# Performance work log

Measured on AMD Instinct MI355X. Metric: run time of the kernel, lower is better.

Reference implementation:

```python
import jax, jax.numpy as jnp
import numpy as np

# model constants (ModelArgs defaults, 7B config)
H, D, BS = 32, 128, 8          # heads, head_dim, sparse_block_size
DIM = H * D                     # 4096
SINK_TOK, WIN_TOK, HEAVY = 60, 60, 1160
MB = HEAVY // BS                # 145 top blocks
T_CTX = 16384                   # prefilled context length


def apply_rope(x, freqs):
    # x: [B,S,H,D], freqs: [S, D//2, 2] -> rotate pairs as in apply_rotary_emb
    B, S, Hh, Dd = x.shape
    xs = x.reshape(B, S, Hh, Dd // 2, 2)
    fc = freqs.reshape(1, S, 1, Dd // 2, 2)
    xr, xi = xs[..., 0], xs[..., 1]
    fr, fi = fc[..., 0], fc[..., 1]
    out = jnp.stack([xr * fr - xi * fi, xi * fr + xr * fi], axis=-1)
    return out.reshape(B, S, Hh, Dd)


def setup_inputs() -> dict:
    key = jax.random.key(0)
    ks = jax.random.split(key, 6)
    B = 1
    return {
        'x': jax.random.normal(ks[0], (B, 1, DIM), jnp.float32),
        'freqs_cis': jax.random.normal(ks[1], (1, D // 2, 2), jnp.float32),
        'wqkv': jax.random.normal(ks[2], (3 * DIM, DIM), jnp.float32) * 0.02,
        'wo': jax.random.normal(ks[3], (DIM, DIM), jnp.float32) * 0.02,
        'k_cache': jax.random.normal(ks[4], (B, H, T_CTX, D), jnp.float32),
        'v_cache': jax.random.normal(ks[5], (B, H, T_CTX, D), jnp.float32),
        'input_pos': T_CTX - 1,
    }


def reference(x, freqs_cis, wqkv, wo, k_cache, v_cache, input_pos):
    B, S, _ = x.shape  # decode step, S == 1
    qkv = x @ wqkv.T                                   # [B,S,3*DIM]
    q, k, v = jnp.split(qkv, [DIM, 2 * DIM], axis=-1)
    q = q.reshape(B, S, H, D)
    k = k.reshape(B, S, H, D)
    v = v.reshape(B, S, H, D)
    q = apply_rope(q, freqs_cis)
    k = apply_rope(k, freqs_cis)

    # KV cache update at input_pos (token layout [B,H,T,D])
    k_bhsd = k.transpose(0, 2, 1, 3)
    v_bhsd = v.transpose(0, 2, 1, 3)
    kc = jax.lax.dynamic_update_slice(k_cache, k_bhsd, (0, 0, input_pos, 0))
    vc = jax.lax.dynamic_update_slice(v_cache, v_bhsd, (0, 0, input_pos, 0))

    T = input_pos + 1            # python int -> static
    Tb = T // BS                 # full blocks (T divisible by BS here)
    scale = 1.0 / np.sqrt(D).astype(np.float32)

    # block representative keys (k_sum_blk / k_cnt_blk mean) and routing scores
    k_mean = kc[:, :, :T].reshape(B, H, Tb, BS, D).mean(axis=3)   # [B,H,Tb,D]
    q1 = q[:, -1]                                                 # [B,H,D]
    scores = jnp.einsum('bhd,bhtd->bht', q1, k_mean) * scale      # [B,H,Tb]

    # build_block_index: sink + window + topk-Mb (static sizes)
    sink_b = min(-(-min(SINK_TOK, T) // BS), Tb)
    window_b = min(-(-min(WIN_TOK, T) // BS), Tb)
    cur_block = (T - 1) // BS
    win_start = max(0, cur_block - window_b + 1)
    win_end = cur_block + 1
    NEG = jnp.float32(-1e30)
    tb = jnp.arange(Tb)
    excl = (tb < sink_b) | ((tb >= win_start) & (tb < win_end))
    _, top_ids = jax.lax.top_k(jnp.where(excl, NEG, scores), MB)  # [B,H,MB]
    sink_ids = jnp.broadcast_to(jnp.arange(sink_b, dtype=jnp.int32), (B, H, sink_b))
    win_ids = jnp.broadcast_to(jnp.arange(win_start, win_end, dtype=jnp.int32), (B, H, win_end - win_start))
    block_index = jnp.concatenate([sink_ids, win_ids, top_ids.astype(jnp.int32)], axis=-1)  # [B,H,KLIST]

    # gather selected blocks' tokens and run restricted attention
    tok = (block_index[..., None] * BS + jnp.arange(BS, dtype=jnp.int32)).reshape(B, H, -1)  # [B,H,N]
    N = tok.shape[-1]
    valid = tok <= input_pos
    tok_c = jnp.clip(tok, 0, T - 1).astype(jnp.int32)
    idx = jnp.broadcast_to(tok_c[..., None], (B, H, N, D))
    k_sel = jnp.take_along_axis(kc, idx, axis=2)                  # [B,H,N,D]
    v_sel = jnp.take_along_axis(vc, idx, axis=2)
    att = jnp.einsum('bhd,bhnd->bhn', q1, k_sel) * scale
    p = jax.nn.softmax(jnp.where(valid, att, NEG), axis=-1)
    out = jnp.einsum('bhn,bhnd->bhd', p, v_sel)                   # [B,H,D]
    y = out.reshape(B, 1, DIM) @ wo.T                             # [B,1,DIM]
    return y
```

## Files before the change

### kernel.cpp

```cpp
#include <hip/hip_runtime.h>
#include <hip/hip_bf16.h>

#define NH 32
#define DH 128
#define DIMM 4096
#define TCTX 16384
#define BSZ 8
#define NBLK_TOT (TCTX / BSZ)
#define MB_SEL 145
#define SINK_TOK 60
#define WIN_TOK 60
#define BLK_CAP 192
#define NSPLIT 27
#define CHUNK 6
#define PSTRIDE (DH + 2)
#define KV_WGS 1024
#define SC_WG_PER_H 128
#define SC_WGS (NH * SC_WG_PER_H)

typedef __attribute__((ext_vector_type(4))) float f4v;

__device__ __forceinline__ float4 ntload4(const float* p) {
    f4v v = __builtin_nontemporal_load((const f4v*)p);
    return make_float4(v.x, v.y, v.z, v.w);
}

__device__ __forceinline__ void gemv_row2(const float* __restrict__ wr0,
                                          const float* __restrict__ wr1,
                                          const float* __restrict__ x, int lane,
                                          float& o0, float& o1) {
    float a0 = 0.f, a1 = 0.f;
    #pragma unroll
    for (int it = 0; it < 16; ++it) {
        int j = lane * 4 + it * 256;
        float4 xv = *(const float4*)(x + j);
        float4 w0 = ntload4(wr0 + j);
        float4 w1 = ntload4(wr1 + j);
        a0 += w0.x * xv.x + w0.y * xv.y + w0.z * xv.z + w0.w * xv.w;
        a1 += w1.x * xv.x + w1.y * xv.y + w1.z * xv.z + w1.w * xv.w;
    }
    #pragma unroll
    for (int m = 1; m < 64; m <<= 1) {
        a0 += __shfl_xor(a0, m, 64);
        a1 += __shfl_xor(a1, m, 64);
    }
    o0 = a0; o1 = a1;
}

__global__ __launch_bounds__(256) void k_q(const float* __restrict__ x,
                                           const float* __restrict__ w,
                                           const float* __restrict__ freqs,
                                           float* __restrict__ q1) {
    int t = threadIdx.x;
    int wave = t >> 6, lane = t & 63;
    int r0 = blockIdx.x * 8 + wave * 2;
    float a0, a1;
    gemv_row2(w + (size_t)r0 * DIMM, w + (size_t)(r0 + 1) * DIMM, x, lane, a0, a1);
    if (lane == 0) {
        int m = (r0 >> 1) & 63;
        float fr = freqs[2 * m], fi = freqs[2 * m + 1];
        float2 o; o.x = a0 * fr - a1 * fi; o.y = a1 * fr + a0 * fi;
        *(float2*)(q1 + r0) = o;
    }
}

__global__ __launch_bounds__(256) void k_mid(const float* __restrict__ x,
                                             const float* __restrict__ w,
                                             const float* __restrict__ freqs,
                                             const float* __restrict__ q1,
                                             const float* __restrict__ kc,
                                             const int* __restrict__ ip_p,
                                             float* __restrict__ kn,
                                             float* __restrict__ vn,
                                             float* __restrict__ scores) {
    int t = threadIdx.x, wave = t >> 6, lane = t & 63;

    if (blockIdx.x < KV_WGS) {
        int r0 = DIMM + blockIdx.x * 8 + wave * 2;
        float a0, a1;
        gemv_row2(w + (size_t)r0 * DIMM, w + (size_t)(r0 + 1) * DIMM, x, lane, a0, a1);
        if (lane == 0) {
            if (r0 < 2 * DIMM) {
                int m = (r0 >> 1) & 63;
                float fr = freqs[2 * m], fi = freqs[2 * m + 1];
                float2 o; o.x = a0 * fr - a1 * fi; o.y = a1 * fr + a0 * fi;
                *(float2*)(kn + (r0 - DIMM)) = o;
            } else {
                float2 o; o.x = a0; o.y = a1;
                *(float2*)(vn + (r0 - 2 * DIMM)) = o;
            }
        }
        return;
    }

    int ip = *ip_p;
    int T = ip + 1;
    int Tb = T / BSZ;
    int sidx = blockIdx.x - KV_WGS;
    int h = sidx >> 7;
    int wg = sidx & 127;
    int b0 = wg * 16 + wave * 4;
    int d0 = (lane * 4) & 127;
    float4 q4 = *(const float4*)(q1 + h * DH + d0);
    const float* kb = kc + ((size_t)h * TCTX + (size_t)b0 * BSZ) * DH;
    float acc[4] = {0.f, 0.f, 0.f, 0.f};
    #pragma unroll
    for (int i = 0; i < 16; ++i) {
        float4 k4 = *(const float4*)(kb + lane * 4 + i * 256);
        acc[i >> 2] += q4.x * k4.x + q4.y * k4.y + q4.z * k4.z + q4.w * k4.w;
    }
    #pragma unroll
    for (int m = 1; m < 64; m <<= 1) {
        acc[0] += __shfl_xor(acc[0], m, 64);
        acc[1] += __shfl_xor(acc[1], m, 64);
        acc[2] += __shfl_xor(acc[2], m, 64);
        acc[3] += __shfl_xor(acc[3], m, 64);
    }
    if (lane == 0) {
        float4 out;
        out.x = (b0 + 0 < Tb) ? acc[0] * 0.011048543456039805f : -1e30f;
        out.y = (b0 + 1 < Tb) ? acc[1] * 0.011048543456039805f : -1e30f;
        out.z = (b0 + 2 < Tb) ? acc[2] * 0.011048543456039805f : -1e30f;
        out.w = (b0 + 3 < Tb) ? acc[3] * 0.011048543456039805f : -1e30f;
        *(float4*)(scores + h * NBLK_TOT + b0) = out;
    }
}

__global__ __launch_bounds__(64) void k_topk(const float* __restrict__ scores,
                                             const int* __restrict__ ip_p,
                                             int* __restrict__ blklist) {
    int h = blockIdx.x;
    int lane = threadIdx.x & 63;
    int ip = *ip_p;
    int T = ip + 1;
    int Tb = T / BSZ;
    int sink_b = min((min(SINK_TOK, T) + BSZ - 1) / BSZ, Tb);
    int window_b = min((min(WIN_TOK, T) + BSZ - 1) / BSZ, Tb);
    int cur = (T - 1) / BSZ;
    int win_start = max(0, cur - window_b + 1);
    int win_end = cur + 1;

    unsigned int u[32];
    const float* sh = scores + h * NBLK_TOT;
    #pragma unroll
    for (int i = 0; i < 32; i += 4) {
        float4 sv = *(const float4*)(sh + lane * 32 + i);
        float fv[4] = {sv.x, sv.y, sv.z, sv.w};
        #pragma unroll
        for (int q = 0; q < 4; ++q) {
            int j = lane * 32 + i + q;
            unsigned int b = __float_as_uint(fv[q]);
            unsigned int m = (b & 0x80000000u) ? ~b : (b | 0x80000000u);
            bool ok = (j < Tb) && (j >= sink_b) && !(j >= win_start && j < win_end);
            u[i + q] = ok ? m : 0u;
        }
    }

    unsigned int lo = 0u, hi = 0xFFFFFFFFu;
    while (lo < hi) {
        unsigned int mid =
            (unsigned int)(((unsigned long long)lo + (unsigned long long)hi + 1ull) >> 1);
        int c = 0;
        #pragma unroll
        for (int i = 0; i < 32; ++i) c += (u[i] >= mid);
        #pragma unroll
        for (int m = 1; m < 64; m <<= 1) c += __shfl_xor(c, m, 64);
        if (c >= MB_SEL) lo = mid; else hi = mid - 1;
    }

    int gt = 0, eq = 0;
    #pragma unroll
    for (int i = 0; i < 32; ++i) { gt += (u[i] > lo); eq += (u[i] == lo); }
    unsigned int packed = ((unsigned int)gt << 16) | (unsigned int)eq;
    unsigned int sc = packed;
    #pragma unroll
    for (int off = 1; off < 64; off <<= 1) {
        unsigned int v = __shfl_up(sc, off, 64);
        if (lane >= off) sc += v;
    }
    unsigned int tot = __shfl(sc, 63, 64);
    unsigned int totg = tot >> 16;
    unsigned int excl = sc - packed;
    int gi = (int)(excl >> 16);
    int ei = (int)(excl & 0xFFFFu);
    int need_eq = MB_SEL - (int)totg;

    int base = sink_b + (win_end - win_start);
    int* bl = blklist + h * BLK_CAP;
    for (int i = lane; i < base; i += 64)
        bl[i] = (i < sink_b) ? i : (win_start + (i - sink_b));

    #pragma unroll
    for (int i = 0; i < 32; ++i) {
        int j = lane * 32 + i;
        if (u[i] > lo) {
            bl[base + gi] = j; ++gi;
        } else if (u[i] == lo) {
            if (ei < need_eq) bl[base + (int)totg + ei] = j;
            ++ei;
        }
    }
}

__global__ __launch_bounds__(256) void k_attn_part(const float* __restrict__ q1,
                                                   const float* __restrict__ kc,
                                                   const float* __restrict__ vc,
                                                   const float* __restrict__ kn,
                                                   const float* __restrict__ vn,
                                                   const int* __restrict__ blklist,
                                                   const int* __restrict__ ip_p,
                                                   float* __restrict__ part) {
    __shared__ float oacc[4][DH];
    __shared__ float2 ml_s[4];
    int h = blockIdx.x / NSPLIT;
    int sp = blockIdx.x % NSPLIT;
    int t = threadIdx.x, wave = t >> 6, lane = t & 63;
    int g = lane >> 4, sub = lane & 15;
    int ip = *ip_p;
    int T = ip + 1;
    int Tb = T / BSZ;
    int sink_b = min((min(SINK_TOK, T) + BSZ - 1) / BSZ, Tb);
    int window_b = min((min(WIN_TOK, T) + BSZ - 1) / BSZ, Tb);
    int cur = (T - 1) / BSZ;
    int win_start = max(0, cur - window_b + 1);
    int nwin = cur + 1 - win_start;
    int nblk = sink_b + nwin + MB_SEL;
    int b0 = sp * CHUNK;
    int nb = min(nblk - b0, CHUNK);
    float* pp = part + ((size_t)h * NSPLIT + sp) * PSTRIDE;
    if (nb <= 0) {
        if (t < DH) pp[t] = 0.f;
        if (t == DH) pp[DH] = -1e30f;
        if (t == DH + 1) pp[DH + 1] = 0.f;
        return;
    }

    float4 qa = *(const float4*)(q1 + h * DH + sub * 8);
    float4 qb = *(const float4*)(q1 + h * DH + sub * 8 + 4);
    const float* kh = kc + (size_t)h * TCTX * DH;
    const float* vh = vc + (size_t)h * TCTX * DH;
    const int* bl = blklist + h * BLK_CAP + b0;

    float m = -1e30f, l = 0.f;
    float4 aa = make_float4(0, 0, 0, 0), ab = make_float4(0, 0, 0, 0);

    for (int c = wave; c < nb * 2; c += 4) {
        int blk = bl[c >> 1];
        int tok = blk * BSZ + (c & 1) * 4 + g;
        const float* kr = (tok == ip) ? (kn + h * DH) : (kh + (size_t)tok * DH);
        const float* vr = (tok == ip) ? (vn + h * DH) : (vh + (size_t)tok * DH);
        float4 ka  = *(const float4*)(kr + sub * 8);
        float4 kb2 = *(const float4*)(kr + sub * 8 + 4);
        float4 va  = *(const float4*)(vr + sub * 8);
        float4 vb  = *(const float4*)(vr + sub * 8 + 4);
        float s = qa.x * ka.x + qa.y * ka.y + qa.z * ka.z + qa.w * ka.w +
                  qb.x * kb2.x + qb.y * kb2.y + qb.z * kb2.z + qb.w * kb2.w;
        s += __shfl_xor(s, 1, 64);
        s += __shfl_xor(s, 2, 64);
        s += __shfl_xor(s, 4, 64);
        s += __shfl_xor(s, 8, 64);
        s *= 0.08838834764831845f;
        float mn = fmaxf(m, s);
        float cf = __expf(m - mn);
        float w  = __expf(s - mn);
        l = l * cf + w;
        aa.x = aa.x * cf + w * va.x; aa.y = aa.y * cf + w * va.y;
        aa.z = aa.z * cf + w * va.z; aa.w = aa.w * cf + w * va.w;
        ab.x = ab.x * cf + w * vb.x; ab.y = ab.y * cf + w * vb.y;
        ab.z = ab.z * cf + w * vb.z; ab.w = ab.w * cf + w * vb.w;
        m = mn;
    }

    #pragma unroll
    for (int off = 16; off < 64; off <<= 1) {
        float mo = __shfl_xor(m, off, 64);
        float lo_ = __shfl_xor(l, off, 64);
        float4 oa, ob;
        oa.x = __shfl_xor(aa.x, off, 64); oa.y = __shfl_xor(aa.y, off, 64);
        oa.z = __shfl_xor(aa.z, off, 64); oa.w = __shfl_xor(aa.w, off, 64);
        ob.x = __shfl_xor(ab.x, off, 64); ob.y = __shfl_xor(ab.y, off, 64);
        ob.z = __shfl_xor(ab.z, off, 64); ob.w = __shfl_xor(ab.w, off, 64);
        float mn = fmaxf(m, mo);
        float c1 = __expf(m - mn), c2 = __expf(mo - mn);
        l = l * c1 + lo_ * c2;
        aa.x = aa.x * c1 + oa.x * c2; aa.y = aa.y * c1 + oa.y * c2;
        aa.z = aa.z * c1 + oa.z * c2; aa.w = aa.w * c1 + oa.w * c2;
        ab.x = ab.x * c1 + ob.x * c2; ab.y = ab.y * c1 + ob.y * c2;
        ab.z = ab.z * c1 + ob.z * c2; ab.w = ab.w * c1 + ob.w * c2;
        m = mn;
    }

    if (g == 0) {
        oacc[wave][sub * 8 + 0] = aa.x; oacc[wave][sub * 8 + 1] = aa.y;
        oacc[wave][sub * 8 + 2] = aa.z; oacc[wave][sub * 8 + 3] = aa.w;
        oacc[wave][sub * 8 + 4] = ab.x; oacc[wave][sub * 8 + 5] = ab.y;
        oacc[wave][sub * 8 + 6] = ab.z; oacc[wave][sub * 8 + 7] = ab.w;
    }
    if (lane == 0) ml_s[wave] = make_float2(m, l);
    __syncthreads();

    if (t < DH + 2) {
        float M = fmaxf(fmaxf(ml_s[0].x, ml_s[1].x), fmaxf(ml_s[2].x, ml_s[3].x));
        float L = 0.f, acc = 0.f;
        #pragma unroll
        for (int wv = 0; wv < 4; ++wv) {
            float cw = __expf(ml_s[wv].x - M);
            L += ml_s[wv].y * cw;
            if (t < DH) acc += oacc[wv][t] * cw;
        }
        if (t < DH) pp[t] = acc;
        else if (t == DH) pp[DH] = M;
        else pp[DH + 1] = L;
    }
}

__global__ __launch_bounds__(128) void k_attn_reduce(const float* __restrict__ part,
                                                     float* __restrict__ o) {
    int h = blockIdx.x, t = threadIdx.x;
    const float* ph = part + (size_t)h * NSPLIT * PSTRIDE;
    float M = -1e30f;
    #pragma unroll 9
    for (int s = 0; s < NSPLIT; ++s) M = fmaxf(M, ph[s * PSTRIDE + DH]);
    float L = 0.f, acc = 0.f;
    #pragma unroll 9
    for (int s = 0; s < NSPLIT; ++s) {
        float w = __expf(ph[s * PSTRIDE + DH] - M);
        L += ph[s * PSTRIDE + DH + 1] * w;
        acc += ph[s * PSTRIDE + t] * w;
    }
    o[h * DH + t] = acc / L;
}

__global__ __launch_bounds__(256) void k_gemv_o(const float* __restrict__ x,
                                                const float* __restrict__ w,
                                                float* __restrict__ out) {
    int t = threadIdx.x;
    int wave = t >> 6, lane = t & 63;
    int r0 = blockIdx.x * 8 + wave * 2;
    float a0, a1;
    gemv_row2(w + (size_t)r0 * DIMM, w + (size_t)(r0 + 1) * DIMM, x, lane, a0, a1);
    if (lane == 0) {
        float2 o; o.x = a0; o.y = a1;
        *(float2*)(out + r0) = o;
    }
}

extern "C" void kernel_launch(void* const* d_in, const int* in_sizes, int n_in,
                              void* d_out, int out_size, void* d_ws, size_t ws_size,
                              hipStream_t stream) {
    const float* x     = (const float*)d_in[0];
    const float* freqs = (const float*)d_in[1];
    const float* wqkv  = (const float*)d_in[2];
    const float* wo    = (const float*)d_in[3];
    const float* kc    = (const float*)d_in[4];
    const float* vc    = (const float*)d_in[5];
    const int*   ip    = (const int*)d_in[6];
    float* y = (float*)d_out;

    float* ws     = (float*)d_ws;
    float* q1     = ws;
    float* kn     = ws + 4096;
    float* vn     = ws + 8192;
    float* scores = ws + 12288;
    float* part   = ws + 77824;
    float* o      = ws + 190144;
    int*   blkl   = (int*)(ws + 194240);

    k_q<<<DIMM / 8, 256, 0, stream>>>(x, wqkv, freqs, q1);
    k_mid<<<KV_WGS + SC_WGS, 256, 0, stream>>>(x, wqkv, freqs, q1, kc, ip,
                                               kn, vn, scores);
    k_topk<<<NH, 64, 0, stream>>>(scores, ip, blkl);
    k_attn_part<<<NH * NSPLIT, 256, 0, stream>>>(q1, kc, vc, kn, vn, blkl, ip, part);
    k_attn_reduce<<<NH, 128, 0, stream>>>(part, o);
    k_gemv_o<<<DIMM / 8, 256, 0, stream>>>(o, wo, y);
}
```

Measured before the change: 124.3 us.

## Fuse top-k selection and split reduction into the attention kernel

```diff
diff --git a/kernel.cpp b/kernel.cpp
--- a/kernel.cpp
+++ b/kernel.cpp
@@ -50,8 +50,10 @@
 __global__ __launch_bounds__(256) void k_q(const float* __restrict__ x,
                                            const float* __restrict__ w,
                                            const float* __restrict__ freqs,
-                                           float* __restrict__ q1) {
+                                           float* __restrict__ q1,
+                                           unsigned int* __restrict__ cnts) {
     int t = threadIdx.x;
+    if (blockIdx.x == 0 && t < NH) cnts[t * 16] = 0u;
     int wave = t >> 6, lane = t & 63;
     int r0 = blockIdx.x * 8 + wave * 2;
     float a0, a1;
@@ -126,92 +128,20 @@
     }
 }
 
-__global__ __launch_bounds__(64) void k_topk(const float* __restrict__ scores,
-                                             const int* __restrict__ ip_p,
-                                             int* __restrict__ blklist) {
-    int h = blockIdx.x;
-    int lane = threadIdx.x & 63;
-    int ip = *ip_p;
-    int T = ip + 1;
-    int Tb = T / BSZ;
-    int sink_b = min((min(SINK_TOK, T) + BSZ - 1) / BSZ, Tb);
-    int window_b = min((min(WIN_TOK, T) + BSZ - 1) / BSZ, Tb);
-    int cur = (T - 1) / BSZ;
-    int win_start = max(0, cur - window_b + 1);
-    int win_end = cur + 1;
-
-    unsigned int u[32];
-    const float* sh = scores + h * NBLK_TOT;
-    #pragma unroll
-    for (int i = 0; i < 32; i += 4) {
-        float4 sv = *(const float4*)(sh + lane * 32 + i);
-        float fv[4] = {sv.x, sv.y, sv.z, sv.w};
-        #pragma unroll
-        for (int q = 0; q < 4; ++q) {
-            int j = lane * 32 + i + q;
-            unsigned int b = __float_as_uint(fv[q]);
-            unsigned int m = (b & 0x80000000u) ? ~b : (b | 0x80000000u);
-            bool ok = (j < Tb) && (j >= sink_b) && !(j >= win_start && j < win_end);
-            u[i + q] = ok ? m : 0u;
-        }
-    }
-
-    unsigned int lo = 0u, hi = 0xFFFFFFFFu;
-    while (lo < hi) {
-        unsigned int mid =
-            (unsigned int)(((unsigned long long)lo + (unsigned long long)hi + 1ull) >> 1);
-        int c = 0;
-        #pragma unroll
-        for (int i = 0; i < 32; ++i) c += (u[i] >= mid);
-        #pragma unroll
-        for (int m = 1; m < 64; m <<= 1) c += __shfl_xor(c, m, 64);
-        if (c >= MB_SEL) lo = mid; else hi = mid - 1;
-    }
-
-    int gt = 0, eq = 0;
-    #pragma unroll
-    for (int i = 0; i < 32; ++i) { gt += (u[i] > lo); eq += (u[i] == lo); }
-    unsigned int packed = ((unsigned int)gt << 16) | (unsigned int)eq;
-    unsigned int sc = packed;
-    #pragma unroll
-    for (int off = 1; off < 64; off <<= 1) {
-        unsigned int v = __shfl_up(sc, off, 64);
-        if (lane >= off) sc += v;
-    }
-    unsigned int tot = __shfl(sc, 63, 64);
-    unsigned int totg = tot >> 16;
-    unsigned int excl = sc - packed;
-    int gi = (int)(excl >> 16);
-    int ei = (int)(excl & 0xFFFFu);
-    int need_eq = MB_SEL - (int)totg;
-
-    int base = sink_b + (win_end - win_start);
-    int* bl = blklist + h * BLK_CAP;
-    for (int i = lane; i < base; i += 64)
-        bl[i] = (i < sink_b) ? i : (win_start + (i - sink_b));
-
-    #pragma unroll
-    for (int i = 0; i < 32; ++i) {
-        int j = lane * 32 + i;
-        if (u[i] > lo) {
-            bl[base + gi] = j; ++gi;
-        } else if (u[i] == lo) {
-            if (ei < need_eq) bl[base + (int)totg + ei] = j;
-            ++ei;
-        }
-    }
-}
-
-__global__ __launch_bounds__(256) void k_attn_part(const float* __restrict__ q1,
-                                                   const float* __restrict__ kc,
-                                                   const float* __restrict__ vc,
-                                                   const float* __restrict__ kn,
-                                                   const float* __restrict__ vn,
-                                                   const int* __restrict__ blklist,
-                                                   const int* __restrict__ ip_p,
-                                                   float* __restrict__ part) {
+__global__ __launch_bounds__(256) void k_attn(const float* __restrict__ q1,
+                                              const float* __restrict__ kc,
+                                              const float* __restrict__ vc,
+                                              const float* __restrict__ kn,
+                                              const float* __restrict__ vn,
+                                              const float* __restrict__ scores,
+                                              const int* __restrict__ ip_p,
+                                              float* __restrict__ part,
+                                              float* __restrict__ o,
+                                              unsigned int* __restrict__ cnts) {
+    __shared__ int bl_s[BLK_CAP];
     __shared__ float oacc[4][DH];
     __shared__ float2 ml_s[4];
+    __shared__ int tailflag;
     int h = blockIdx.x / NSPLIT;
     int sp = blockIdx.x % NSPLIT;
     int t = threadIdx.x, wave = t >> 6, lane = t & 63;
@@ -223,29 +153,82 @@
     int window_b = min((min(WIN_TOK, T) + BSZ - 1) / BSZ, Tb);
     int cur = (T - 1) / BSZ;
     int win_start = max(0, cur - window_b + 1);
-    int nwin = cur + 1 - win_start;
+    int win_end = cur + 1;
+    int nwin = win_end - win_start;
     int nblk = sink_b + nwin + MB_SEL;
     int b0 = sp * CHUNK;
     int nb = min(nblk - b0, CHUNK);
     float* pp = part + ((size_t)h * NSPLIT + sp) * PSTRIDE;
-    if (nb <= 0) {
-        if (t < DH) pp[t] = 0.f;
-        if (t == DH) pp[DH] = -1e30f;
-        if (t == DH + 1) pp[DH + 1] = 0.f;
-        return;
-    }
+
+    if (wave == 0) {
+        unsigned int u[32];
+        const float* sh = scores + h * NBLK_TOT;
+        #pragma unroll
+        for (int i = 0; i < 32; i += 4) {
+            float4 sv = *(const float4*)(sh + lane * 32 + i);
+            float fv[4] = {sv.x, sv.y, sv.z, sv.w};
+            #pragma unroll
+            for (int q = 0; q < 4; ++q) {
+                int j = lane * 32 + i + q;
+                unsigned int b = __float_as_uint(fv[q]);
+                unsigned int m = (b & 0x80000000u) ? ~b : (b | 0x80000000u);
+                bool ok = (j < Tb) && (j >= sink_b) && !(j >= win_start && j < win_end);
+                u[i + q] = ok ? m : 0u;
+            }
+        }
+        unsigned int lo = 0u, hi = 0xFFFFFFFFu;
+        while (lo < hi) {
+            unsigned int mid =
+                (unsigned int)(((unsigned long long)lo + (unsigned long long)hi + 1ull) >> 1);
+            int c = 0;
+            #pragma unroll
+            for (int i = 0; i < 32; ++i) c += (u[i] >= mid);
+            #pragma unroll
+            for (int m = 1; m < 64; m <<= 1) c += __shfl_xor(c, m, 64);
+            if (c >= MB_SEL) lo = mid; else hi = mid - 1;
+        }
+        int gt = 0, eq = 0;
+        #pragma unroll
+        for (int i = 0; i < 32; ++i) { gt += (u[i] > lo); eq += (u[i] == lo); }
+        unsigned int packed = ((unsigned int)gt << 16) | (unsigned int)eq;
+        unsigned int sc = packed;
+        #pragma unroll
+        for (int off = 1; off < 64; off <<= 1) {
+            unsigned int v = __shfl_up(sc, off, 64);
+            if (lane >= off) sc += v;
+        }
+        unsigned int tot = __shfl(sc, 63, 64);
+        unsigned int totg = tot >> 16;
+        unsigned int excl = sc - packed;
+        int gi = (int)(excl >> 16);
+        int ei = (int)(excl & 0xFFFFu);
+        int need_eq = MB_SEL - (int)totg;
+        int base = sink_b + nwin;
+        for (int i = lane; i < base; i += 64)
+            bl_s[i] = (i < sink_b) ? i : (win_start + (i - sink_b));
+        #pragma unroll
+        for (int i = 0; i < 32; ++i) {
+            int j = lane * 32 + i;
+            if (u[i] > lo) {
+                bl_s[base + gi] = j; ++gi;
+            } else if (u[i] == lo) {
+                if (ei < need_eq) bl_s[base + (int)totg + ei] = j;
+                ++ei;
+            }
+        }
+    }
+    __syncthreads();
 
     float4 qa = *(const float4*)(q1 + h * DH + sub * 8);
     float4 qb = *(const float4*)(q1 + h * DH + sub * 8 + 4);
     const float* kh = kc + (size_t)h * TCTX * DH;
     const float* vh = vc + (size_t)h * TCTX * DH;
-    const int* bl = blklist + h * BLK_CAP + b0;
 
     float m = -1e30f, l = 0.f;
     float4 aa = make_float4(0, 0, 0, 0), ab = make_float4(0, 0, 0, 0);
 
     for (int c = wave; c < nb * 2; c += 4) {
-        int blk = bl[c >> 1];
+        int blk = bl_s[b0 + (c >> 1)];
         int tok = blk * BSZ + (c & 1) * 4 + g;
         const float* kr = (tok == ip) ? (kn + h * DH) : (kh + (size_t)tok * DH);
         const float* vr = (tok == ip) ? (vn + h * DH) : (vh + (size_t)tok * DH);
@@ -312,23 +295,27 @@
         else if (t == DH) pp[DH] = M;
         else pp[DH + 1] = L;
     }
-}
-
-__global__ __launch_bounds__(128) void k_attn_reduce(const float* __restrict__ part,
-                                                     float* __restrict__ o) {
-    int h = blockIdx.x, t = threadIdx.x;
-    const float* ph = part + (size_t)h * NSPLIT * PSTRIDE;
-    float M = -1e30f;
-    #pragma unroll 9
-    for (int s = 0; s < NSPLIT; ++s) M = fmaxf(M, ph[s * PSTRIDE + DH]);
-    float L = 0.f, acc = 0.f;
-    #pragma unroll 9
-    for (int s = 0; s < NSPLIT; ++s) {
-        float w = __expf(ph[s * PSTRIDE + DH] - M);
-        L += ph[s * PSTRIDE + DH + 1] * w;
-        acc += ph[s * PSTRIDE + t] * w;
-    }
-    o[h * DH + t] = acc / L;
+
+    __syncthreads();
+    if (t == 0) {
+        __threadfence();
+        unsigned int old = atomicAdd(&cnts[h * 16], 1u);
+        tailflag = (old == NSPLIT - 1) ? 1 : 0;
+    }
+    __syncthreads();
+    if (tailflag && t < DH) {
+        __threadfence();
+        const float* ph = part + (size_t)h * NSPLIT * PSTRIDE;
+        float M = -1e30f;
+        for (int s = 0; s < NSPLIT; ++s) M = fmaxf(M, ph[s * PSTRIDE + DH]);
+        float L = 0.f, acc = 0.f;
+        for (int s = 0; s < NSPLIT; ++s) {
+            float w = __expf(ph[s * PSTRIDE + DH] - M);
+            L += ph[s * PSTRIDE + DH + 1] * w;
+            acc += ph[s * PSTRIDE + t] * w;
+        }
+        o[h * DH + t] = acc / L;
+    }
 }
 
 __global__ __launch_bounds__(256) void k_gemv_o(const float* __restrict__ x,
@@ -364,13 +351,12 @@
     float* scores = ws + 12288;
     float* part   = ws + 77824;
     float* o      = ws + 190144;
-    int*   blkl   = (int*)(ws + 194240);
-
-    k_q<<<DIMM / 8, 256, 0, stream>>>(x, wqkv, freqs, q1);
+    unsigned int* cnts = (unsigned int*)(ws + 194240);
+
+    k_q<<<DIMM / 8, 256, 0, stream>>>(x, wqkv, freqs, q1, cnts);
     k_mid<<<KV_WGS + SC_WGS, 256, 0, stream>>>(x, wqkv, freqs, q1, kc, ip,
                                                kn, vn, scores);
-    k_topk<<<NH, 64, 0, stream>>>(scores, ip, blkl);
-    k_attn_part<<<NH * NSPLIT, 256, 0, stream>>>(q1, kc, vc, kn, vn, blkl, ip, part);
-    k_attn_reduce<<<NH, 128, 0, stream>>>(part, o);
+    k_attn<<<NH * NSPLIT, 256, 0, stream>>>(q1, kc, vc, kn, vn, scores, ip,
+                                            part, o, cnts);
     k_gemv_o<<<DIMM / 8, 256, 0, stream>>>(o, wo, y);
 }
```

Result: slower. 152.9 us (+23.0%).
